# Kernel tuning notes

Hardware: AMD Instinct MI355X
Metric: run time of the kernel (lower is better)

Reference implementation:

```python
import jax, jax.numpy as jnp
import numpy as np

NODE_DIM, MSG_DIM, PROP_DIM, HIDDEN = 64, 64, 32, 128
V, T, S = 10000, 8, 16


def setup_inputs() -> dict:
    key = jax.random.key(0)
    ks = jax.random.split(key, 8)
    in_dim = NODE_DIM + MSG_DIM + 1 + PROP_DIM  # concat width of the attn MLP
    return {
        "h_t": jax.random.normal(ks[0], (V, NODE_DIM), dtype=jnp.float32),
        "messages": jax.random.normal(ks[1], (V, T, S, MSG_DIM), dtype=jnp.float32),
        "tau_values": jax.random.uniform(ks[2], (T,), dtype=jnp.float32),
        "theta": jax.random.normal(ks[3], (V, PROP_DIM), dtype=jnp.float32),
        "W1": jax.random.normal(ks[4], (in_dim, HIDDEN), dtype=jnp.float32) * 0.02,
        "b1": jnp.zeros((HIDDEN,), dtype=jnp.float32),
        "W2": jax.random.normal(ks[5], (HIDDEN, 1), dtype=jnp.float32) * 0.02,
        "b2": jnp.zeros((1,), dtype=jnp.float32),
    }


def reference(h_t, messages, tau_values, theta, W1, b1, W2, b2):
    # Equivalent to concat([h_exp, messages, tau_exp, theta_exp]) @ W1:
    # split W1 by input block and sum the partial projections, avoiding the
    # materialized (V, T, S, node+msg+1+prop) broadcast-concat tensor.
    Wh = W1[:NODE_DIM]                                  # (node_dim, H)
    Wm = W1[NODE_DIM:NODE_DIM + MSG_DIM]                # (msg_dim, H)
    Wt = W1[NODE_DIM + MSG_DIM]                         # (H,) -- the tau row
    Wp = W1[NODE_DIM + MSG_DIM + 1:]                    # (prop_dim, H)

    hidden = (
        jnp.einsum("vtsd,dh->vtsh", messages, Wm)       # (V, T, S, H)
        + (h_t @ Wh)[:, None, None, :]                  # broadcast over T, S
        + tau_values[None, :, None, None] * Wt[None, None, None, :]
        + (theta @ Wp)[:, None, None, :]
        + b1
    )
    hidden = jax.nn.relu(hidden)
    logits = (hidden @ W2 + b2)[..., 0]                 # (V, T, S)
    return logits
```

## Files before the change

kernel.cpp:

```cpp
#include <hip/hip_runtime.h>
#include <hip/hip_bf16.h>

#define VN 10000
#define HID 128

using bf16x8 = __attribute__((ext_vector_type(8))) __bf16;
using f32x4  = __attribute__((ext_vector_type(4))) float;

typedef const __attribute__((address_space(1))) uint32_t gbl_u32;
typedef __attribute__((address_space(3))) uint32_t lds_u32;

__global__ __launch_bounds__(256) void prep_kernel(
    const float* __restrict__ h_t, const float* __restrict__ theta,
    const float* __restrict__ W1, const float* __restrict__ b1,
    float* __restrict__ base, __bf16* __restrict__ wmt)
{
  const int blk = blockIdx.x;
  const int tid = threadIdx.x;
  if (blk < 625) {
    __shared__ __align__(16) float in[16][96];
    const int v0 = blk * 16;
    {
      const float4* src = (const float4*)(h_t + (size_t)v0 * 64);
      float4 f = src[tid];
      int vl = tid >> 4, c = (tid & 15) * 4;
      *(float4*)&in[vl][c] = f;
    }
    if (tid < 128) {
      const float4* src = (const float4*)(theta + (size_t)v0 * 32);
      float4 f = src[tid];
      int vl = tid >> 3, c = 64 + (tid & 7) * 4;
      *(float4*)&in[vl][c] = f;
    }
    __syncthreads();
    const int h = tid & 127;
    const int half = tid >> 7;
    float acc[8];
    const float bb = b1[h];
    #pragma unroll
    for (int k = 0; k < 8; k++) acc[k] = bb;
    #pragma unroll 4
    for (int dc = 0; dc < 16; dc++) {
      const int d = 4 * dc;
      float w0 = W1[(d + 0) * 128 + h];
      float w1 = W1[(d + 1) * 128 + h];
      float w2 = W1[(d + 2) * 128 + h];
      float w3 = W1[(d + 3) * 128 + h];
      #pragma unroll
      for (int k = 0; k < 8; k++) {
        float4 iv = *(const float4*)&in[2 * k + half][d];
        acc[k] += iv.x * w0 + iv.y * w1 + iv.z * w2 + iv.w * w3;
      }
    }
    #pragma unroll 4
    for (int dc = 0; dc < 8; dc++) {
      const int d = 4 * dc;
      float w0 = W1[(129 + d + 0) * 128 + h];
      float w1 = W1[(129 + d + 1) * 128 + h];
      float w2 = W1[(129 + d + 2) * 128 + h];
      float w3 = W1[(129 + d + 3) * 128 + h];
      #pragma unroll
      for (int k = 0; k < 8; k++) {
        float4 iv = *(const float4*)&in[2 * k + half][64 + d];
        acc[k] += iv.x * w0 + iv.y * w1 + iv.z * w2 + iv.w * w3;
      }
    }
    #pragma unroll
    for (int k = 0; k < 8; k++)
      base[(size_t)(v0 + 2 * k + half) * 128 + h] = acc[k];
  } else {
    int j = (blk - 625) * 256 + tid;
    int n = j >> 6, d = j & 63;
    wmt[j] = (__bf16)W1[(64 + d) * 128 + n];
  }
}

__global__ __launch_bounds__(256, 3) void main_kernel(
    const float* __restrict__ messages, const float* __restrict__ tau,
    const float* __restrict__ W1, const float* __restrict__ W2,
    const float* __restrict__ b2, const float* __restrict__ base,
    const __bf16* __restrict__ wmt, float* __restrict__ out)
{
  __shared__ __align__(16) unsigned char lds[33280 + 18432 + 512];
  __bf16* lB = (__bf16*)(lds + 33280);
  float* lOut = (float*)(lds + 33280 + 18432);

  const int v = blockIdx.x;
  const int tid = threadIdx.x;
  const int w = tid >> 6;
  const int lane = tid & 63;
  const int quad = lane >> 4;
  const int l16 = lane & 15;

  const float* msg = messages + (size_t)v * 8192;

  uint4 breg[4];
  {
    const uint4* bsrc = (const uint4*)wmt;
    #pragma unroll
    for (int j = 0; j < 4; j++) breg[j] = bsrc[j * 256 + tid];
  }

  #pragma unroll
  for (int j = 0; j < 8; j++) {
    const float* g = msg + (32 * w + 4 * j) * 64 + lane * 4;
    __builtin_amdgcn_global_load_lds((gbl_u32*)g,
                                     (lds_u32*)(lds + w * 8320 + j * 1040),
                                     16, 0, 0);
  }

  float bb[8], w2v[8], wtv[8];
  #pragma unroll
  for (int nt = 0; nt < 8; nt++) {
    const int n = nt * 16 + l16;
    bb[nt]  = base[(size_t)v * 128 + n];
    w2v[nt] = W2[n];
    wtv[nt] = W1[128 * 128 + n];
  }
  float tv[2];
  tv[0] = tau[2 * w];
  tv[1] = tau[2 * w + 1];
  const float b2v = b2[0];

  #pragma unroll
  for (int j = 0; j < 4; j++) {
    int idx = j * 256 + tid;
    int r = idx >> 3, c = (idx & 7) * 8;
    *(uint4*)&lB[r * 72 + c] = breg[j];
  }

  __syncthreads();

  f32x4 acc[2][8];
  #pragma unroll
  for (int mt = 0; mt < 2; mt++)
    #pragma unroll
    for (int nt = 0; nt < 8; nt++) acc[mt][nt] = (f32x4){0.f, 0.f, 0.f, 0.f};

  #pragma unroll
  for (int ks = 0; ks < 2; ks++) {
    bf16x8 b[8];
    #pragma unroll
    for (int nt = 0; nt < 8; nt++)
      b[nt] = *(const bf16x8*)&lB[(nt * 16 + l16) * 72 + ks * 32 + quad * 8];
    #pragma unroll
    for (int mt = 0; mt < 2; mt++) {
      const int rr = mt * 16 + l16;
      const float4* ap = (const float4*)(lds + w * 8320 + (rr >> 2) * 1040 +
                                         (rr & 3) * 256 + (ks * 32 + quad * 8) * 4);
      float4 f0 = ap[0], f1 = ap[1];
      bf16x8 a;
      a[0] = (__bf16)f0.x; a[1] = (__bf16)f0.y; a[2] = (__bf16)f0.z; a[3] = (__bf16)f0.w;
      a[4] = (__bf16)f1.x; a[5] = (__bf16)f1.y; a[6] = (__bf16)f1.z; a[7] = (__bf16)f1.w;
      #pragma unroll
      for (int nt = 0; nt < 8; nt++)
        acc[mt][nt] = __builtin_amdgcn_mfma_f32_16x16x32_bf16(a, b[nt], acc[mt][nt], 0, 0, 0);
    }
  }

  #pragma unroll
  for (int mt = 0; mt < 2; mt++) {
    float ps[4] = {0.f, 0.f, 0.f, 0.f};
    #pragma unroll
    for (int nt = 0; nt < 8; nt++) {
      const float add = bb[nt] + tv[mt] * wtv[nt];
      f32x4 a4 = acc[mt][nt];
      #pragma unroll
      for (int r = 0; r < 4; r++) {
        float hdn = fmaxf(a4[r] + add, 0.f);
        ps[r] += hdn * w2v[nt];
      }
    }
    #pragma unroll
    for (int off = 1; off < 16; off <<= 1)
      #pragma unroll
      for (int r = 0; r < 4; r++) ps[r] += __shfl_xor(ps[r], off, 64);
    if (l16 == 0) {
      #pragma unroll
      for (int r = 0; r < 4; r++)
        lOut[32 * w + mt * 16 + quad * 4 + r] = ps[r];
    }
  }
  __syncthreads();
  if (tid < 128) out[(size_t)v * 128 + tid] = lOut[tid] + b2v;
}

extern "C" void kernel_launch(void* const* d_in, const int* in_sizes, int n_in,
                              void* d_out, int out_size, void* d_ws, size_t ws_size,
                              hipStream_t stream) {
  const float* h_t      = (const float*)d_in[0];
  const float* messages = (const float*)d_in[1];
  const float* tau      = (const float*)d_in[2];
  const float* theta    = (const float*)d_in[3];
  const float* W1       = (const float*)d_in[4];
  const float* b1       = (const float*)d_in[5];
  const float* W2       = (const float*)d_in[6];
  const float* b2       = (const float*)d_in[7];
  float* out = (float*)d_out;

  float* base = (float*)d_ws;
  __bf16* wmt = (__bf16*)((char*)d_ws + (size_t)VN * HID * sizeof(float));

  prep_kernel<<<625 + 32, 256, 0, stream>>>(h_t, theta, W1, b1, base, wmt);
  main_kernel<<<VN, 256, 0, stream>>>(messages, tau, W1, W2, b2, base, wmt, out);
}
```

Baseline: 456.0 us.

## Make main kernel persistent with register-resident weights and double-buffered message prefetch

Replaces the one-block-per-node launch with a persistent grid of 512 blocks. Each block keeps the bf16 W_m fragments in registers and loops over nodes, prefetching the next node's messages and base values into registers while computing the current one. LDS staging, the barriers and the LDS output buffer go away, and results are written straight to global memory. The intent is to hide memory latency on this bandwidth-bound kernel and avoid per-block setup, at the cost of higher register pressure and only 512 blocks of parallelism (launch bounds lowered to 2).

```diff
diff --git a/kernel.cpp b/kernel.cpp
--- a/kernel.cpp
+++ b/kernel.cpp
@@ -3,12 +3,10 @@
 
 #define VN 10000
 #define HID 128
+#define GRID_MAIN 512
 
 using bf16x8 = __attribute__((ext_vector_type(8))) __bf16;
 using f32x4  = __attribute__((ext_vector_type(4))) float;
-
-typedef const __attribute__((address_space(1))) uint32_t gbl_u32;
-typedef __attribute__((address_space(3))) uint32_t lds_u32;
 
 __global__ __launch_bounds__(256) void prep_kernel(
     const float* __restrict__ h_t, const float* __restrict__ theta,
@@ -75,114 +73,112 @@
   }
 }
 
-__global__ __launch_bounds__(256, 3) void main_kernel(
+__global__ __launch_bounds__(256, 2) void main_kernel(
     const float* __restrict__ messages, const float* __restrict__ tau,
     const float* __restrict__ W1, const float* __restrict__ W2,
     const float* __restrict__ b2, const float* __restrict__ base,
     const __bf16* __restrict__ wmt, float* __restrict__ out)
 {
-  __shared__ __align__(16) unsigned char lds[33280 + 18432 + 512];
-  __bf16* lB = (__bf16*)(lds + 33280);
-  float* lOut = (float*)(lds + 33280 + 18432);
-
-  const int v = blockIdx.x;
-  const int tid = threadIdx.x;
-  const int w = tid >> 6;
+  const int tid  = threadIdx.x;
+  const int w    = tid >> 6;
   const int lane = tid & 63;
   const int quad = lane >> 4;
-  const int l16 = lane & 15;
-
-  const float* msg = messages + (size_t)v * 8192;
-
-  uint4 breg[4];
-  {
-    const uint4* bsrc = (const uint4*)wmt;
-    #pragma unroll
-    for (int j = 0; j < 4; j++) breg[j] = bsrc[j * 256 + tid];
-  }
-
+  const int l16  = lane & 15;
+  const int rowbase = 32 * w;
+
+  bf16x8 Bf[2][8];
   #pragma unroll
-  for (int j = 0; j < 8; j++) {
-    const float* g = msg + (32 * w + 4 * j) * 64 + lane * 4;
-    __builtin_amdgcn_global_load_lds((gbl_u32*)g,
-                                     (lds_u32*)(lds + w * 8320 + j * 1040),
-                                     16, 0, 0);
-  }
-
-  float bb[8], w2v[8], wtv[8];
+  for (int ks = 0; ks < 2; ks++)
+    #pragma unroll
+    for (int nt = 0; nt < 8; nt++)
+      Bf[ks][nt] = *(const bf16x8*)(wmt + (nt * 16 + l16) * 64 + ks * 32 + quad * 8);
+
+  float w2v[8], wtv[8];
   #pragma unroll
   for (int nt = 0; nt < 8; nt++) {
     const int n = nt * 16 + l16;
-    bb[nt]  = base[(size_t)v * 128 + n];
     w2v[nt] = W2[n];
     wtv[nt] = W1[128 * 128 + n];
   }
-  float tv[2];
-  tv[0] = tau[2 * w];
-  tv[1] = tau[2 * w + 1];
+  const float tv0 = tau[2 * w];
+  const float tv1 = tau[2 * w + 1];
   const float b2v = b2[0];
 
-  #pragma unroll
-  for (int j = 0; j < 4; j++) {
-    int idx = j * 256 + tid;
-    int r = idx >> 3, c = (idx & 7) * 8;
-    *(uint4*)&lB[r * 72 + c] = breg[j];
+  auto PREF = [&](int v, f32x4 (&A)[2][2][2], float (&bb)[8]) {
+    const float* msg = messages + (size_t)v * 8192;
+    #pragma unroll
+    for (int mt = 0; mt < 2; mt++)
+      #pragma unroll
+      for (int ks = 0; ks < 2; ks++) {
+        const float* p = msg + (rowbase + mt * 16 + l16) * 64 + ks * 32 + quad * 8;
+        A[mt][ks][0] = *(const f32x4*)p;
+        A[mt][ks][1] = *(const f32x4*)(p + 4);
+      }
+    #pragma unroll
+    for (int nt = 0; nt < 8; nt++)
+      bb[nt] = base[(size_t)v * 128 + nt * 16 + l16];
+  };
+
+  auto COMP = [&](int v, const f32x4 (&A)[2][2][2], const float (&bb)[8]) {
+    bf16x8 af[2][2];
+    #pragma unroll
+    for (int mt = 0; mt < 2; mt++)
+      #pragma unroll
+      for (int ks = 0; ks < 2; ks++)
+        #pragma unroll
+        for (int j = 0; j < 4; j++) {
+          af[mt][ks][j]     = (__bf16)A[mt][ks][0][j];
+          af[mt][ks][4 + j] = (__bf16)A[mt][ks][1][j];
+        }
+    float ps0[4] = {0.f, 0.f, 0.f, 0.f};
+    float ps1[4] = {0.f, 0.f, 0.f, 0.f};
+    #pragma unroll
+    for (int nt = 0; nt < 8; nt++) {
+      f32x4 acc0 = (f32x4){0.f, 0.f, 0.f, 0.f};
+      f32x4 acc1 = (f32x4){0.f, 0.f, 0.f, 0.f};
+      acc0 = __builtin_amdgcn_mfma_f32_16x16x32_bf16(af[0][0], Bf[0][nt], acc0, 0, 0, 0);
+      acc0 = __builtin_amdgcn_mfma_f32_16x16x32_bf16(af[0][1], Bf[1][nt], acc0, 0, 0, 0);
+      acc1 = __builtin_amdgcn_mfma_f32_16x16x32_bf16(af[1][0], Bf[0][nt], acc1, 0, 0, 0);
+      acc1 = __builtin_amdgcn_mfma_f32_16x16x32_bf16(af[1][1], Bf[1][nt], acc1, 0, 0, 0);
+      const float add0 = bb[nt] + tv0 * wtv[nt];
+      const float add1 = bb[nt] + tv1 * wtv[nt];
+      #pragma unroll
+      for (int r = 0; r < 4; r++) {
+        ps0[r] += fmaxf(acc0[r] + add0, 0.f) * w2v[nt];
+        ps1[r] += fmaxf(acc1[r] + add1, 0.f) * w2v[nt];
+      }
+    }
+    #pragma unroll
+    for (int off = 1; off < 16; off <<= 1)
+      #pragma unroll
+      for (int r = 0; r < 4; r++) {
+        ps0[r] += __shfl_xor(ps0[r], off, 64);
+        ps1[r] += __shfl_xor(ps1[r], off, 64);
+      }
+    if (l16 == 0) {
+      f32x4 o0, o1;
+      #pragma unroll
+      for (int r = 0; r < 4; r++) { o0[r] = ps0[r] + b2v; o1[r] = ps1[r] + b2v; }
+      *(f32x4*)&out[(size_t)v * 128 + rowbase + quad * 4]      = o0;
+      *(f32x4*)&out[(size_t)v * 128 + rowbase + 16 + quad * 4] = o1;
+    }
+  };
+
+  f32x4 A0[2][2][2], A1[2][2][2];
+  float bb0[8], bb1[8];
+  int v = blockIdx.x;
+  PREF(v, A0, bb0);
+  while (true) {
+    const int v1 = v + GRID_MAIN;
+    if (v1 < VN) PREF(v1, A1, bb1);
+    COMP(v, A0, bb0);
+    if (v1 >= VN) break;
+    const int v2 = v1 + GRID_MAIN;
+    if (v2 < VN) PREF(v2, A0, bb0);
+    COMP(v1, A1, bb1);
+    if (v2 >= VN) break;
+    v = v2;
   }
-
-  __syncthreads();
-
-  f32x4 acc[2][8];
-  #pragma unroll
-  for (int mt = 0; mt < 2; mt++)
-    #pragma unroll
-    for (int nt = 0; nt < 8; nt++) acc[mt][nt] = (f32x4){0.f, 0.f, 0.f, 0.f};
-
-  #pragma unroll
-  for (int ks = 0; ks < 2; ks++) {
-    bf16x8 b[8];
-    #pragma unroll
-    for (int nt = 0; nt < 8; nt++)
-      b[nt] = *(const bf16x8*)&lB[(nt * 16 + l16) * 72 + ks * 32 + quad * 8];
-    #pragma unroll
-    for (int mt = 0; mt < 2; mt++) {
-      const int rr = mt * 16 + l16;
-      const float4* ap = (const float4*)(lds + w * 8320 + (rr >> 2) * 1040 +
-                                         (rr & 3) * 256 + (ks * 32 + quad * 8) * 4);
-      float4 f0 = ap[0], f1 = ap[1];
-      bf16x8 a;
-      a[0] = (__bf16)f0.x; a[1] = (__bf16)f0.y; a[2] = (__bf16)f0.z; a[3] = (__bf16)f0.w;
-      a[4] = (__bf16)f1.x; a[5] = (__bf16)f1.y; a[6] = (__bf16)f1.z; a[7] = (__bf16)f1.w;
-      #pragma unroll
-      for (int nt = 0; nt < 8; nt++)
-        acc[mt][nt] = __builtin_amdgcn_mfma_f32_16x16x32_bf16(a, b[nt], acc[mt][nt], 0, 0, 0);
-    }
-  }
-
-  #pragma unroll
-  for (int mt = 0; mt < 2; mt++) {
-    float ps[4] = {0.f, 0.f, 0.f, 0.f};
-    #pragma unroll
-    for (int nt = 0; nt < 8; nt++) {
-      const float add = bb[nt] + tv[mt] * wtv[nt];
-      f32x4 a4 = acc[mt][nt];
-      #pragma unroll
-      for (int r = 0; r < 4; r++) {
-        float hdn = fmaxf(a4[r] + add, 0.f);
-        ps[r] += hdn * w2v[nt];
-      }
-    }
-    #pragma unroll
-    for (int off = 1; off < 16; off <<= 1)
-      #pragma unroll
-      for (int r = 0; r < 4; r++) ps[r] += __shfl_xor(ps[r], off, 64);
-    if (l16 == 0) {
-      #pragma unroll
-      for (int r = 0; r < 4; r++)
-        lOut[32 * w + mt * 16 + quad * 4 + r] = ps[r];
-    }
-  }
-  __syncthreads();
-  if (tid < 128) out[(size_t)v * 128 + tid] = lOut[tid] + b2v;
 }
 
 extern "C" void kernel_launch(void* const* d_in, const int* in_sizes, int n_in,
@@ -202,5 +198,5 @@
   __bf16* wmt = (__bf16*)((char*)d_ws + (size_t)VN * HID * sizeof(float));
 
   prep_kernel<<<625 + 32, 256, 0, stream>>>(h_t, theta, W1, b1, base, wmt);
-  main_kernel<<<VN, 256, 0, stream>>>(messages, tau, W1, W2, b2, base, wmt, out);
+  main_kernel<<<GRID_MAIN, 256, 0, stream>>>(messages, tau, W1, W2, b2, base, wmt, out);
 }
```

New measurement: 463.8 us. About the same (+1.7%).
